# Optimization experiments

Hardware: AMD Instinct MI355X
Metric: run time of the kernel (lower is better)

## Reference

```python
import jax, jax.numpy as jnp
import numpy as np
import math

B, NH, SQ, HD = 4, 32, 512, 128
MLEN = 3584


def setup_inputs() -> dict:
    key = jax.random.key(0)
    k1, k2, k3, k4 = jax.random.split(key, 4)
    q = jax.random.normal(k1, (B, NH, SQ, HD), dtype=jnp.float32)
    k = jax.random.normal(k2, (B, NH, SQ, HD), dtype=jnp.float32)
    v = jax.random.normal(k3, (B, NH, SQ, HD), dtype=jnp.float32)
    mem = jax.random.normal(k4, (B, MLEN, 2 * NH * HD), dtype=jnp.float32)
    mask = jnp.ones((B, 1, SQ, MLEN + SQ), dtype=jnp.float32)
    return {"q": q, "k": k, "v": v, "mask": mask, "mem": mem}


def reference(q, k, v, mask, mem):
    b, nh, sq, hd = k.shape
    mlen = mem.shape[1]
    # cache_kv: stack (k,v) -> (2,b,nh,sq,hd), permute -> (b,sq,2,nh,hd), flatten
    cache_kv = jnp.stack((k, v)).transpose(1, 3, 0, 2, 4).reshape(b, sq, 2 * nh * hd)
    # split cached mem into memk/memv: (b,mlen,2,nh,hd) -> (2,b,nh,mlen,hd)
    mem_r = mem.reshape(b, mlen, 2, nh, hd).transpose(2, 0, 3, 1, 4)
    k_full = jnp.concatenate([mem_r[0], k], axis=2)  # [b,nh,mlen+sq,hd]
    v_full = jnp.concatenate([mem_r[1], v], axis=2)
    scale = 1.0 / math.sqrt(hd)
    scores = jnp.einsum("bhqd,bhkd->bhqk", q * scale, k_full)
    # standard_attention general mask path (mask.shape[-2] != 1)
    scores = scores * mask - 10000.0 * (1.0 - mask)
    probs = jax.nn.softmax(scores, axis=-1)
    context = jnp.einsum("bhqk,bhkd->bhqd", probs, v_full)
    return context, cache_kv
```

## Files before the change

### kernel.cpp

```cpp
#include <hip/hip_runtime.h>

#define B_ 4
#define NH_ 32
#define SQ_ 512
#define HD_ 128
#define MLEN_ 3584
#define KT_ 4096
#define QB_ 128
#define KB_ 32
#define NTILE_ 128
#define MEMTILES_ 112

typedef float f32x4 __attribute__((ext_vector_type(4)));
typedef short s16x8 __attribute__((ext_vector_type(8)));

__device__ __forceinline__ f32x4 MFMA16(s16x8 a, s16x8 b, f32x4 c) {
    return __builtin_amdgcn_mfma_f32_16x16x32_bf16(a, b, c, 0, 0, 0);
}

__device__ __forceinline__ s16x8 cvt8(float4 a, float4 b) {
    union { s16x8 v; __bf16 h[8]; } u;
    u.h[0] = (__bf16)a.x; u.h[1] = (__bf16)a.y;
    u.h[2] = (__bf16)a.z; u.h[3] = (__bf16)a.w;
    u.h[4] = (__bf16)b.x; u.h[5] = (__bf16)b.y;
    u.h[6] = (__bf16)b.z; u.h[7] = (__bf16)b.w;
    return u.v;
}

__launch_bounds__(256, 2)
__global__ void attn_kernel(const float* __restrict__ q, const float* __restrict__ k,
                            const float* __restrict__ v, const float* __restrict__ mask,
                            const float* __restrict__ mem, float* __restrict__ ctx)
{
    __shared__ __bf16 Kb[2][KB_ * HD_];
    __shared__ __bf16 Vtb[2][HD_ * KB_];

    const int tid  = threadIdx.x;
    const int lane = tid & 63;
    const int w    = tid >> 6;
    const int l15  = lane & 15;
    const int l4   = lane >> 4;
    const int xv   = (lane & 7) << 4;

    const int qt   = blockIdx.x >> 7;
    const int pair = blockIdx.x & 127;
    const int b    = pair >> 5;
    const int h    = pair & 31;
    const int q0   = qt * QB_;

    const float scale = 0.088388347648318447f;
    s16x8 qf[2][4];
    {
        const float* qbase = q + (((size_t)(b * NH_ + h)) * SQ_ + q0 + w * 32 + l15) * HD_;
        #pragma unroll
        for (int m = 0; m < 2; ++m)
            #pragma unroll
            for (int kc = 0; kc < 4; ++kc) {
                const float* p = qbase + (size_t)m * 16 * HD_ + kc * 32 + l4 * 8;
                float4 a = *(const float4*)p;
                float4 c = *(const float4*)(p + 4);
                a.x *= scale; a.y *= scale; a.z *= scale; a.w *= scale;
                c.x *= scale; c.y *= scale; c.z *= scale; c.w *= scale;
                qf[m][kc] = cvt8(a, c);
            }
    }

    f32x4 acc[2][8];
    #pragma unroll
    for (int m = 0; m < 2; ++m)
        #pragma unroll
        for (int n = 0; n < 8; ++n) acc[m][n] = (f32x4){0.f, 0.f, 0.f, 0.f};

    float mrun[2] = {-3.0e38f, -3.0e38f}, lrun[2] = {0.f, 0.f};

    const float* maskrow = mask + ((size_t)b * SQ_ + q0 + w * 32 + l15) * KT_;

    const int krow = tid >> 4,  kcg  = tid & 15;
    const int vhd  = tid & 127, vkvb = tid >> 7;
    const int vsw  = (vhd >> 1) & 3;

    {
        const float* mrow = mem + ((size_t)b * MLEN_) * (2 * NH_ * HD_) + h * HD_;
        const float* srcK = mrow;
        const float* srcV = mrow + NH_ * HD_;
        const int rs = 2 * NH_ * HD_;
        #pragma unroll
        for (int it = 0; it < 2; ++it) {
            int row = krow + it * 16;
            const float* p = srcK + (size_t)row * rs + kcg * 8;
            float4 a = *(const float4*)p;
            float4 c = *(const float4*)(p + 4);
            int byte = row * 256 + ((kcg * 16) ^ ((row & 7) << 4));
            *(s16x8*)((char*)Kb[0] + byte) = cvt8(a, c);
        }
        #pragma unroll
        for (int it = 0; it < 2; ++it) {
            int kvb = vkvb + it * 2;
            const float* p = srcV + (size_t)(kvb * 8) * rs + vhd;
            union { s16x8 v; __bf16 hh[8]; } u;
            #pragma unroll
            for (int j = 0; j < 8; ++j) u.hh[j] = (__bf16)p[(size_t)j * rs];
            int byte = vhd * 64 + (((kvb ^ vsw) & 3) << 4);
            *(s16x8*)((char*)Vtb[0] + byte) = u.v;
        }
    }
    __syncthreads();

    for (int t = 0; t < NTILE_; ++t) {
        const int cur = t & 1;
        const int kv0 = t * KB_;
        const bool havenext = (t + 1 < NTILE_);

        f32x4 mk[2][2];
        #pragma unroll
        for (int m = 0; m < 2; ++m)
            #pragma unroll
            for (int mt = 0; mt < 2; ++mt)
                mk[m][mt] = *(const f32x4*)(maskrow + (size_t)m * 16 * KT_ +
                                            kv0 + mt * 16 + l4 * 4);

        float4 ka0, kb0, ka1, kb1;
        float vp0[8], vp1[8];
        if (havenext) {
            const float *srcK, *srcV; int rs;
            const int nkv0 = (t + 1) * KB_;
            if (t + 1 < MEMTILES_) {
                const float* mrow = mem + ((size_t)b * MLEN_ + nkv0) * (2 * NH_ * HD_) + h * HD_;
                srcK = mrow; srcV = mrow + NH_ * HD_; rs = 2 * NH_ * HD_;
            } else {
                size_t off = (((size_t)b * NH_ + h) * SQ_ + (nkv0 - MLEN_)) * HD_;
                srcK = k + off; srcV = v + off; rs = HD_;
            }
            const float* p0 = srcK + (size_t)krow * rs + kcg * 8;
            ka0 = *(const float4*)p0; kb0 = *(const float4*)(p0 + 4);
            const float* p1 = srcK + (size_t)(krow + 16) * rs + kcg * 8;
            ka1 = *(const float4*)p1; kb1 = *(const float4*)(p1 + 4);
            const float* q0p = srcV + (size_t)(vkvb * 8) * rs + vhd;
            #pragma unroll
            for (int j = 0; j < 8; ++j) vp0[j] = q0p[(size_t)j * rs];
            const float* q1p = srcV + (size_t)((vkvb + 2) * 8) * rs + vhd;
            #pragma unroll
            for (int j = 0; j < 8; ++j) vp1[j] = q1p[(size_t)j * rs];
        }

        f32x4 st[2][2];
        st[0][0] = (f32x4){0.f,0.f,0.f,0.f}; st[0][1] = (f32x4){0.f,0.f,0.f,0.f};
        st[1][0] = (f32x4){0.f,0.f,0.f,0.f}; st[1][1] = (f32x4){0.f,0.f,0.f,0.f};
        __builtin_amdgcn_s_setprio(1);
        #pragma unroll
        for (int mt = 0; mt < 2; ++mt) {
            #pragma unroll
            for (int kc = 0; kc < 4; ++kc) {
                s16x8 kf = *(const s16x8*)((const char*)Kb[cur] +
                            (mt * 16 + l15) * 256 + (((kc * 4 + l4) * 16) ^ xv));
                st[0][mt] = MFMA16(kf, qf[0][kc], st[0][mt]);
                st[1][mt] = MFMA16(kf, qf[1][kc], st[1][mt]);
            }
        }
        __builtin_amdgcn_s_setprio(0);

        s16x8 pa[2];
        #pragma unroll
        for (int m = 0; m < 2; ++m) {
            #pragma unroll
            for (int mt = 0; mt < 2; ++mt)
                #pragma unroll
                for (int r = 0; r < 4; ++r)
                    st[m][mt][r] = fmaf(mk[m][mt][r], st[m][mt][r] + 10000.f, -10000.f);

            float rm = fmaxf(fmaxf(fmaxf(st[m][0][0], st[m][0][1]),
                                   fmaxf(st[m][0][2], st[m][0][3])),
                             fmaxf(fmaxf(st[m][1][0], st[m][1][1]),
                                   fmaxf(st[m][1][2], st[m][1][3])));
            rm = fmaxf(rm, __shfl_xor(rm, 16));
            rm = fmaxf(rm, __shfl_xor(rm, 32));

            if (!__all(rm <= mrun[m] + 8.f)) {
                float nm = fmaxf(mrun[m], rm);
                float al = __expf(mrun[m] - nm);
                mrun[m] = nm;
                lrun[m] *= al;
                float a0 = __shfl(al, l4 * 4 + 0);
                float a1 = __shfl(al, l4 * 4 + 1);
                float a2 = __shfl(al, l4 * 4 + 2);
                float a3 = __shfl(al, l4 * 4 + 3);
                #pragma unroll
                for (int nn = 0; nn < 8; ++nn) {
                    acc[m][nn][0] *= a0; acc[m][nn][1] *= a1;
                    acc[m][nn][2] *= a2; acc[m][nn][3] *= a3;
                }
            }

            float rs = 0.f;
            #pragma unroll
            for (int mt = 0; mt < 2; ++mt)
                #pragma unroll
                for (int r = 0; r < 4; ++r) {
                    float pe = __expf(st[m][mt][r] - mrun[m]);
                    st[m][mt][r] = pe;
                    rs += pe;
                }
            rs += __shfl_xor(rs, 16);
            rs += __shfl_xor(rs, 32);
            lrun[m] += rs;

            union PK { int d[2]; __bf16 hh[4]; };
            PK pk0, pk1;
            pk0.hh[0]=(__bf16)st[m][0][0]; pk0.hh[1]=(__bf16)st[m][0][1];
            pk0.hh[2]=(__bf16)st[m][0][2]; pk0.hh[3]=(__bf16)st[m][0][3];
            pk1.hh[0]=(__bf16)st[m][1][0]; pk1.hh[1]=(__bf16)st[m][1][1];
            pk1.hh[2]=(__bf16)st[m][1][2]; pk1.hh[3]=(__bf16)st[m][1][3];

            const int srcA = (l4 & 1) * 32 + l15;
            const int srcB = srcA + 16;
            const int sel  = l4 >> 1;
            union { int d[4]; s16x8 v; } ua;
            int a0 = __shfl(pk0.d[0], srcA), a1 = __shfl(pk0.d[1], srcA);
            int b0 = __shfl(pk1.d[0], srcA), b1 = __shfl(pk1.d[1], srcA);
            int a2 = __shfl(pk0.d[0], srcB), a3 = __shfl(pk0.d[1], srcB);
            int b2 = __shfl(pk1.d[0], srcB), b3 = __shfl(pk1.d[1], srcB);
            ua.d[0] = sel ? b0 : a0; ua.d[1] = sel ? b1 : a1;
            ua.d[2] = sel ? b2 : a2; ua.d[3] = sel ? b3 : a3;
            pa[m] = ua.v;
        }

        __builtin_amdgcn_s_setprio(1);
        #pragma unroll
        for (int nn = 0; nn < 8; ++nn) {
            int hdv = nn * 16 + l15;
            s16x8 vf = *(const s16x8*)((const char*)Vtb[cur] +
                         hdv * 64 + (((l4 ^ ((hdv >> 1) & 3)) & 3) << 4));
            acc[0][nn] = MFMA16(pa[0], vf, acc[0][nn]);
            acc[1][nn] = MFMA16(pa[1], vf, acc[1][nn]);
        }
        __builtin_amdgcn_s_setprio(0);

        if (havenext) {
            int row0 = krow;
            int by0 = row0 * 256 + ((kcg * 16) ^ ((row0 & 7) << 4));
            *(s16x8*)((char*)Kb[cur ^ 1] + by0) = cvt8(ka0, kb0);
            int row1 = krow + 16;
            int by1 = row1 * 256 + ((kcg * 16) ^ ((row1 & 7) << 4));
            *(s16x8*)((char*)Kb[cur ^ 1] + by1) = cvt8(ka1, kb1);

            union { s16x8 v; __bf16 hh[8]; } u0, u1;
            #pragma unroll
            for (int j = 0; j < 8; ++j) u0.hh[j] = (__bf16)vp0[j];
            int vb0 = vhd * 64 + (((vkvb ^ vsw) & 3) << 4);
            *(s16x8*)((char*)Vtb[cur ^ 1] + vb0) = u0.v;
            #pragma unroll
            for (int j = 0; j < 8; ++j) u1.hh[j] = (__bf16)vp1[j];
            int vb1 = vhd * 64 + ((((vkvb + 2) ^ vsw) & 3) << 4);
            *(s16x8*)((char*)Vtb[cur ^ 1] + vb1) = u1.v;
        }

        __syncthreads();
    }

    #pragma unroll
    for (int m = 0; m < 2; ++m) {
        float lr0 = __shfl(lrun[m], l4 * 4 + 0);
        float lr1 = __shfl(lrun[m], l4 * 4 + 1);
        float lr2 = __shfl(lrun[m], l4 * 4 + 2);
        float lr3 = __shfl(lrun[m], l4 * 4 + 3);
        float i0 = 1.f / lr0, i1 = 1.f / lr1, i2 = 1.f / lr2, i3 = 1.f / lr3;
        float* obase = ctx + (((size_t)(b * NH_ + h)) * SQ_ +
                              q0 + w * 32 + m * 16 + l4 * 4) * HD_ + l15;
        #pragma unroll
        for (int nn = 0; nn < 8; ++nn) {
            obase[(size_t)0 * HD_ + nn * 16] = acc[m][nn][0] * i0;
            obase[(size_t)1 * HD_ + nn * 16] = acc[m][nn][1] * i1;
            obase[(size_t)2 * HD_ + nn * 16] = acc[m][nn][2] * i2;
            obase[(size_t)3 * HD_ + nn * 16] = acc[m][nn][3] * i3;
        }
    }
}

__global__ void cachekv_kernel(const float* __restrict__ k, const float* __restrict__ v,
                               float* __restrict__ out)
{
    size_t i = ((size_t)blockIdx.x * 256 + threadIdx.x) * 4;
    unsigned f = (unsigned)i;
    unsigned d    = f & 127;
    unsigned hh   = (f >> 7) & 31;
    unsigned part = (f >> 12) & 1;
    unsigned s    = (f >> 13) & 511;
    unsigned bb   = f >> 22;
    const float* src = (part ? v : k) + (((size_t)(bb * 32u + hh)) * 512u + s) * 128u + d;
    *(float4*)(out + i) = *(const float4*)src;
}

extern "C" void kernel_launch(void* const* d_in, const int* in_sizes, int n_in,
                              void* d_out, int out_size, void* d_ws, size_t ws_size,
                              hipStream_t stream) {
    const float* q    = (const float*)d_in[0];
    const float* k    = (const float*)d_in[1];
    const float* v    = (const float*)d_in[2];
    const float* mask = (const float*)d_in[3];
    const float* mem  = (const float*)d_in[4];
    float* out = (float*)d_out;

    attn_kernel<<<dim3(B_ * NH_ * (SQ_ / QB_)), dim3(256), 0, stream>>>(q, k, v, mask, mem, out);

    const int ctx_elems = B_ * NH_ * SQ_ * HD_;
    const int ckv_elems = B_ * SQ_ * 2 * NH_ * HD_;
    cachekv_kernel<<<dim3(ckv_elems / 4 / 256), dim3(256), 0, stream>>>(k, v, out + ctx_elems);
    (void)in_sizes; (void)n_in; (void)out_size; (void)d_ws; (void)ws_size;
}
```

Measured before the change: 329.0 us.

## Split KV sequence across two blocks and merge partials in reduce kernel

Splits the key/value sequence into two halves handled by separate blocks, doubling the grid. Each block writes unnormalized partial outputs plus running max and sum, and a new reduce kernel combines them with log-sum-exp rescaling. The double-buffered prefetch of the next K/V tile is removed in favor of single-buffered LDS with two barriers per tile. This exposes more parallelism but loses load/compute overlap and adds an extra pass over partial outputs.

```diff
diff --git a/kernel.cpp b/kernel.cpp
--- a/kernel.cpp
+++ b/kernel.cpp
@@ -10,6 +10,7 @@
 #define KB_ 32
 #define NTILE_ 128
 #define MEMTILES_ 112
+#define HTILES_ 64
 
 typedef float f32x4 __attribute__((ext_vector_type(4)));
 typedef short s16x8 __attribute__((ext_vector_type(8)));
@@ -28,12 +29,13 @@
 }
 
 __launch_bounds__(256, 2)
-__global__ void attn_kernel(const float* __restrict__ q, const float* __restrict__ k,
-                            const float* __restrict__ v, const float* __restrict__ mask,
-                            const float* __restrict__ mem, float* __restrict__ ctx)
+__global__ void attn_split_kernel(const float* __restrict__ q, const float* __restrict__ k,
+                                  const float* __restrict__ v, const float* __restrict__ mask,
+                                  const float* __restrict__ mem,
+                                  float* __restrict__ opart, float2* __restrict__ ml)
 {
-    __shared__ __bf16 Kb[2][KB_ * HD_];
-    __shared__ __bf16 Vtb[2][HD_ * KB_];
+    __shared__ __bf16 Kb[KB_ * HD_];
+    __shared__ __bf16 Vtb[HD_ * KB_];
 
     const int tid  = threadIdx.x;
     const int lane = tid & 63;
@@ -42,11 +44,13 @@
     const int l4   = lane >> 4;
     const int xv   = (lane & 7) << 4;
 
-    const int qt   = blockIdx.x >> 7;
+    const int half = blockIdx.x >> 9;
+    const int qt   = (blockIdx.x >> 7) & 3;
     const int pair = blockIdx.x & 127;
     const int b    = pair >> 5;
     const int h    = pair & 31;
     const int q0   = qt * QB_;
+    const int t0   = half * HTILES_;
 
     const float scale = 0.088388347648318447f;
     s16x8 qf[2][4];
@@ -79,11 +83,24 @@
     const int vhd  = tid & 127, vkvb = tid >> 7;
     const int vsw  = (vhd >> 1) & 3;
 
-    {
-        const float* mrow = mem + ((size_t)b * MLEN_) * (2 * NH_ * HD_) + h * HD_;
-        const float* srcK = mrow;
-        const float* srcV = mrow + NH_ * HD_;
-        const int rs = 2 * NH_ * HD_;
+    for (int t = t0; t < t0 + HTILES_; ++t) {
+        const int kv0 = t * KB_;
+        const float *srcK, *srcV;
+        int rs;
+        if (t < MEMTILES_) {
+            const float* mrow = mem + ((size_t)b * MLEN_ + kv0) * (2 * NH_ * HD_) + h * HD_;
+            srcK = mrow;
+            srcV = mrow + NH_ * HD_;
+            rs = 2 * NH_ * HD_;
+        } else {
+            size_t off = (((size_t)b * NH_ + h) * SQ_ + (kv0 - MLEN_)) * HD_;
+            srcK = k + off;
+            srcV = v + off;
+            rs = HD_;
+        }
+
+        __syncthreads();
+
         #pragma unroll
         for (int it = 0; it < 2; ++it) {
             int row = krow + it * 16;
@@ -91,7 +108,7 @@
             float4 a = *(const float4*)p;
             float4 c = *(const float4*)(p + 4);
             int byte = row * 256 + ((kcg * 16) ^ ((row & 7) << 4));
-            *(s16x8*)((char*)Kb[0] + byte) = cvt8(a, c);
+            *(s16x8*)((char*)Kb + byte) = cvt8(a, c);
         }
         #pragma unroll
         for (int it = 0; it < 2; ++it) {
@@ -101,15 +118,8 @@
             #pragma unroll
             for (int j = 0; j < 8; ++j) u.hh[j] = (__bf16)p[(size_t)j * rs];
             int byte = vhd * 64 + (((kvb ^ vsw) & 3) << 4);
-            *(s16x8*)((char*)Vtb[0] + byte) = u.v;
-        }
-    }
-    __syncthreads();
-
-    for (int t = 0; t < NTILE_; ++t) {
-        const int cur = t & 1;
-        const int kv0 = t * KB_;
-        const bool havenext = (t + 1 < NTILE_);
+            *(s16x8*)((char*)Vtb + byte) = u.v;
+        }
 
         f32x4 mk[2][2];
         #pragma unroll
@@ -119,29 +129,7 @@
                 mk[m][mt] = *(const f32x4*)(maskrow + (size_t)m * 16 * KT_ +
                                             kv0 + mt * 16 + l4 * 4);
 
-        float4 ka0, kb0, ka1, kb1;
-        float vp0[8], vp1[8];
-        if (havenext) {
-            const float *srcK, *srcV; int rs;
-            const int nkv0 = (t + 1) * KB_;
-            if (t + 1 < MEMTILES_) {
-                const float* mrow = mem + ((size_t)b * MLEN_ + nkv0) * (2 * NH_ * HD_) + h * HD_;
-                srcK = mrow; srcV = mrow + NH_ * HD_; rs = 2 * NH_ * HD_;
-            } else {
-                size_t off = (((size_t)b * NH_ + h) * SQ_ + (nkv0 - MLEN_)) * HD_;
-                srcK = k + off; srcV = v + off; rs = HD_;
-            }
-            const float* p0 = srcK + (size_t)krow * rs + kcg * 8;
-            ka0 = *(const float4*)p0; kb0 = *(const float4*)(p0 + 4);
-            const float* p1 = srcK + (size_t)(krow + 16) * rs + kcg * 8;
-            ka1 = *(const float4*)p1; kb1 = *(const float4*)(p1 + 4);
-            const float* q0p = srcV + (size_t)(vkvb * 8) * rs + vhd;
-            #pragma unroll
-            for (int j = 0; j < 8; ++j) vp0[j] = q0p[(size_t)j * rs];
-            const float* q1p = srcV + (size_t)((vkvb + 2) * 8) * rs + vhd;
-            #pragma unroll
-            for (int j = 0; j < 8; ++j) vp1[j] = q1p[(size_t)j * rs];
-        }
+        __syncthreads();
 
         f32x4 st[2][2];
         st[0][0] = (f32x4){0.f,0.f,0.f,0.f}; st[0][1] = (f32x4){0.f,0.f,0.f,0.f};
@@ -151,7 +139,7 @@
         for (int mt = 0; mt < 2; ++mt) {
             #pragma unroll
             for (int kc = 0; kc < 4; ++kc) {
-                s16x8 kf = *(const s16x8*)((const char*)Kb[cur] +
+                s16x8 kf = *(const s16x8*)((const char*)Kb +
                             (mt * 16 + l15) * 256 + (((kc * 4 + l4) * 16) ^ xv));
                 st[0][mt] = MFMA16(kf, qf[0][kc], st[0][mt]);
                 st[1][mt] = MFMA16(kf, qf[1][kc], st[1][mt]);
@@ -191,18 +179,18 @@
                 }
             }
 
-            float rs = 0.f;
+            float rsum = 0.f;
             #pragma unroll
             for (int mt = 0; mt < 2; ++mt)
                 #pragma unroll
                 for (int r = 0; r < 4; ++r) {
                     float pe = __expf(st[m][mt][r] - mrun[m]);
                     st[m][mt][r] = pe;
-                    rs += pe;
+                    rsum += pe;
                 }
-            rs += __shfl_xor(rs, 16);
-            rs += __shfl_xor(rs, 32);
-            lrun[m] += rs;
+            rsum += __shfl_xor(rsum, 16);
+            rsum += __shfl_xor(rsum, 32);
+            lrun[m] += rsum;
 
             union PK { int d[2]; __bf16 hh[4]; };
             PK pk0, pk1;
@@ -228,52 +216,53 @@
         #pragma unroll
         for (int nn = 0; nn < 8; ++nn) {
             int hdv = nn * 16 + l15;
-            s16x8 vf = *(const s16x8*)((const char*)Vtb[cur] +
+            s16x8 vf = *(const s16x8*)((const char*)Vtb +
                          hdv * 64 + (((l4 ^ ((hdv >> 1) & 3)) & 3) << 4));
             acc[0][nn] = MFMA16(pa[0], vf, acc[0][nn]);
             acc[1][nn] = MFMA16(pa[1], vf, acc[1][nn]);
         }
         __builtin_amdgcn_s_setprio(0);
-
-        if (havenext) {
-            int row0 = krow;
-            int by0 = row0 * 256 + ((kcg * 16) ^ ((row0 & 7) << 4));
-            *(s16x8*)((char*)Kb[cur ^ 1] + by0) = cvt8(ka0, kb0);
-            int row1 = krow + 16;
-            int by1 = row1 * 256 + ((kcg * 16) ^ ((row1 & 7) << 4));
-            *(s16x8*)((char*)Kb[cur ^ 1] + by1) = cvt8(ka1, kb1);
-
-            union { s16x8 v; __bf16 hh[8]; } u0, u1;
-            #pragma unroll
-            for (int j = 0; j < 8; ++j) u0.hh[j] = (__bf16)vp0[j];
-            int vb0 = vhd * 64 + (((vkvb ^ vsw) & 3) << 4);
-            *(s16x8*)((char*)Vtb[cur ^ 1] + vb0) = u0.v;
-            #pragma unroll
-            for (int j = 0; j < 8; ++j) u1.hh[j] = (__bf16)vp1[j];
-            int vb1 = vhd * 64 + ((((vkvb + 2) ^ vsw) & 3) << 4);
-            *(s16x8*)((char*)Vtb[cur ^ 1] + vb1) = u1.v;
-        }
-
-        __syncthreads();
     }
 
     #pragma unroll
     for (int m = 0; m < 2; ++m) {
-        float lr0 = __shfl(lrun[m], l4 * 4 + 0);
-        float lr1 = __shfl(lrun[m], l4 * 4 + 1);
-        float lr2 = __shfl(lrun[m], l4 * 4 + 2);
-        float lr3 = __shfl(lrun[m], l4 * 4 + 3);
-        float i0 = 1.f / lr0, i1 = 1.f / lr1, i2 = 1.f / lr2, i3 = 1.f / lr3;
-        float* obase = ctx + (((size_t)(b * NH_ + h)) * SQ_ +
-                              q0 + w * 32 + m * 16 + l4 * 4) * HD_ + l15;
+        float* obase = opart + (size_t)half * (B_ * NH_ * SQ_ * HD_) +
+                       (((size_t)(b * NH_ + h)) * SQ_ +
+                        q0 + w * 32 + m * 16 + l4 * 4) * HD_ + l15;
         #pragma unroll
         for (int nn = 0; nn < 8; ++nn) {
-            obase[(size_t)0 * HD_ + nn * 16] = acc[m][nn][0] * i0;
-            obase[(size_t)1 * HD_ + nn * 16] = acc[m][nn][1] * i1;
-            obase[(size_t)2 * HD_ + nn * 16] = acc[m][nn][2] * i2;
-            obase[(size_t)3 * HD_ + nn * 16] = acc[m][nn][3] * i3;
+            obase[(size_t)0 * HD_ + nn * 16] = acc[m][nn][0];
+            obase[(size_t)1 * HD_ + nn * 16] = acc[m][nn][1];
+            obase[(size_t)2 * HD_ + nn * 16] = acc[m][nn][2];
+            obase[(size_t)3 * HD_ + nn * 16] = acc[m][nn][3];
+        }
+        if (l4 == 0) {
+            int row = (b * NH_ + h) * SQ_ + q0 + w * 32 + m * 16 + l15;
+            ml[half * (B_ * NH_ * SQ_) + row] = make_float2(mrun[m], lrun[m]);
         }
     }
+}
+
+__global__ void reduce_kernel(const float* __restrict__ part, const float2* __restrict__ ml,
+                              float* __restrict__ ctx)
+{
+    int idx = blockIdx.x * 256 + threadIdx.x;
+    int row = idx >> 5;
+    int c4  = (idx & 31) * 4;
+    float2 a = ml[row];
+    float2 c = ml[(B_ * NH_ * SQ_) + row];
+    float mm = fmaxf(a.x, c.x);
+    float e0 = __expf(a.x - mm), e1 = __expf(c.x - mm);
+    float inv = 1.f / (a.y * e0 + c.y * e1);
+    const float4 o0 = *(const float4*)(part + (size_t)row * HD_ + c4);
+    const float4 o1 = *(const float4*)(part + (size_t)(B_ * NH_ * SQ_) * HD_ +
+                                       (size_t)row * HD_ + c4);
+    float4 o;
+    o.x = (o0.x * e0 + o1.x * e1) * inv;
+    o.y = (o0.y * e0 + o1.y * e1) * inv;
+    o.z = (o0.z * e0 + o1.z * e1) * inv;
+    o.w = (o0.w * e0 + o1.w * e1) * inv;
+    *(float4*)(ctx + (size_t)row * HD_ + c4) = o;
 }
 
 __global__ void cachekv_kernel(const float* __restrict__ k, const float* __restrict__ v,
@@ -300,10 +289,18 @@
     const float* mem  = (const float*)d_in[4];
     float* out = (float*)d_out;
 
-    attn_kernel<<<dim3(B_ * NH_ * (SQ_ / QB_)), dim3(256), 0, stream>>>(q, k, v, mask, mem, out);
-
     const int ctx_elems = B_ * NH_ * SQ_ * HD_;
     const int ckv_elems = B_ * SQ_ * 2 * NH_ * HD_;
+
+    float*  part = out + ctx_elems;
+    float2* ml   = (float2*)d_ws;
+
+    attn_split_kernel<<<dim3(2 * B_ * NH_ * (SQ_ / QB_)), dim3(256), 0, stream>>>(
+        q, k, v, mask, mem, part, ml);
+
+    reduce_kernel<<<dim3(ctx_elems / 4 / 256), dim3(256), 0, stream>>>(part, ml, out);
+
     cachekv_kernel<<<dim3(ckv_elems / 4 / 256), dim3(256), 0, stream>>>(k, v, out + ctx_elems);
-    (void)in_sizes; (void)n_in; (void)out_size; (void)d_ws; (void)ws_size;
-}
+
+    (void)in_sizes; (void)n_in; (void)out_size; (void)ws_size;
+}
```

After: 365.8 us. 1.11x slower.
